# Performance work log

Measured on AMD Instinct MI355X. Metric: run time of the kernel, lower is better.

## Reference

```python
import jax, jax.numpy as jnp
import numpy as np

B, C, HK, WK = 1, 128, 32, 32
S = 4                       # upsample factor hq/hk = dilation
HQ, WQ = HK * S, WK * S
NH = 4                      # heads
HD = C // NH                # head dim
KH = KW = 7                 # odd(max(3, round(2*0.1*32)))
DH = DW = S
EPS = float(jnp.finfo(jnp.float32).eps)  # torch RMSNorm default eps for fp32


def natten_indices(L, K, D):
    """NATTEN clamped-window key indices per query position. Returns [L, K] int array."""
    NS = K // 2
    i = np.arange(L)
    if D <= 1:
        start = np.maximum(i - NS, 0) + (i + NS >= L) * (L - i - NS - 1)
    else:
        ni = i - NS * D
        imodd = i % D
        a = (L // D) * D
        b = L - a
        far = np.where(imodd < b, L - b + imodd - 2 * NS * D, a + imodd - K * D)
        start = np.where(ni < 0, imodd, np.where(i + NS * D >= L, far, ni))
    return jnp.asarray(start[:, None] + np.arange(K)[None, :] * D)


def setup_inputs() -> dict:
    key = jax.random.key(0)
    ks = jax.random.split(key, 8)
    sc = 1.0 / np.sqrt(C)
    return {
        "q": jax.random.normal(ks[0], (B, C, HQ, WQ), jnp.float32),
        "k": jax.random.normal(ks[1], (B, C, HK, WK), jnp.float32),
        "v": jax.random.normal(ks[2], (B, C, HK, WK), jnp.float32),
        "conv_w": jax.random.normal(ks[3], (C, C, 3, 3), jnp.float32) * (sc / 3.0),
        "normq_w": 1.0 + 0.02 * jax.random.normal(ks[4], (C,), jnp.float32),
        "normk_w": 1.0 + 0.02 * jax.random.normal(ks[5], (C,), jnp.float32),
        "qproj_w": jax.random.normal(ks[6], (C, C), jnp.float32) * sc,
        "qproj_b": jnp.zeros((C,), jnp.float32),
        "kproj_w": jax.random.normal(ks[7], (C, C), jnp.float32) * sc,
        "kproj_b": jnp.zeros((C,), jnp.float32),
    }


def _rmsnorm(x, w):  # x: [B,C,H,W]; RMS over channel dim
    ms = jnp.mean(x * x, axis=1, keepdims=True)
    return x * jax.lax.rsqrt(ms + EPS) * w[None, :, None, None]


def reference(q, k, v, conv_w, normq_w, normk_w, qproj_w, qproj_b, kproj_w, kproj_b):
    # 3x3 conv on q (no bias, padding=1)
    q = jax.lax.conv_general_dilated(q, conv_w, (1, 1), "SAME",
                                     dimension_numbers=("NCHW", "OIHW", "NCHW"))
    q = _rmsnorm(q, normq_w)
    k = _rmsnorm(k, normk_w)
    # 1x1 projections (Conv2d k=1 with bias)
    q = jnp.einsum("oc,bchw->bohw", qproj_w, q) + qproj_b[None, :, None, None]
    k = jnp.einsum("oc,bchw->bohw", kproj_w, k) + kproj_b[None, :, None, None]
    # nearest-exact upsample of k, v to (HQ, WQ); integer factor -> exact pixel repeat
    k = jnp.repeat(jnp.repeat(k, S, axis=2), S, axis=3)
    v = jnp.repeat(jnp.repeat(v, S, axis=2), S, axis=3)
    # NATTEN layout [B, H, W, heads, hd]
    qn = q.reshape(B, NH, HD, HQ, WQ).transpose(0, 3, 4, 1, 2)
    kn = k.reshape(B, NH, HD, HQ, WQ).transpose(0, 3, 4, 1, 2)
    vh = v.transpose(0, 2, 3, 1)  # [B,HQ,WQ,C]; V is shared (expanded) across heads.
    # channel-pad-to-8 in the original is a no-op here since C % 8 == 0.
    ih = natten_indices(HQ, KH, DH)  # [HQ, KH]
    iw = natten_indices(WQ, KW, DW)  # [WQ, KW]
    k_nb = jnp.take(jnp.take(kn, ih, axis=1), iw, axis=3)  # [B,HQ,KH,WQ,KW,NH,HD]
    v_nb = jnp.take(jnp.take(vh, ih, axis=1), iw, axis=3)  # [B,HQ,KH,WQ,KW,C]
    scale = HD ** -0.5
    logits = jnp.einsum("bijhd,bimjnhd->bijhmn", qn, k_nb) * scale
    attn = jax.nn.softmax(logits.reshape(B, HQ, WQ, NH, KH * KW), axis=-1)
    attn = attn.reshape(B, HQ, WQ, NH, KH, KW)
    # heads share V, and the block takes mean over heads at the end; the mean
    # commutes with the (linear) V-contraction, so average attention first.
    attn_mean = attn.mean(axis=3)  # [B,HQ,WQ,KH,KW]
    out = jnp.einsum("bijmn,bimjnc->bcij", attn_mean, v_nb)  # [B,C,HQ,WQ]
    return out
```

## Files before the change

### kernel.cpp

```cpp
#include <hip/hip_runtime.h>

#define EPS_ 1.1920928955078125e-07f
#define SCALE_ 0.17677669529663687f

typedef __attribute__((ext_vector_type(8))) short s8b;
typedef __attribute__((ext_vector_type(4))) float f32x4;

static __device__ __forceinline__ unsigned short f2bf(float f) {
  unsigned int u = __float_as_uint(f);
  unsigned int r = (u + 0x7fffu + ((u >> 16) & 1u)) >> 16;
  return (unsigned short)r;
}
static __device__ __forceinline__ float b2fs(short h) {
  return __uint_as_float(((unsigned int)(unsigned short)h) << 16);
}
static __device__ __forceinline__ int S_(int c) {
  return (c < 3) ? 0 : ((c > 28) ? 25 : (c - 3));
}

__global__ __launch_bounds__(256) void prep_k(
    const float* __restrict__ q_in, const float* __restrict__ k_in,
    const float* __restrict__ v_in, const float* __restrict__ conv_w,
    const float* __restrict__ normq_w, const float* __restrict__ normk_w,
    const float* __restrict__ qproj_w, const float* __restrict__ kproj_w,
    const float* __restrict__ kbias,
    unsigned short* __restrict__ qb, unsigned short* __restrict__ vb,
    unsigned short* __restrict__ kpb, unsigned short* __restrict__ wb,
    unsigned short* __restrict__ wnq) {
  __shared__ __align__(16) char smem[53504];
  unsigned short* t_l = (unsigned short*)smem;
  unsigned short* x_l = (unsigned short*)smem;
  unsigned short* wnk_l = (unsigned short*)(smem + 17408);
  float* red_l = (float*)(smem + 52224);
  float* rs_l  = (float*)(smem + 53248);
  const int b = blockIdx.x, tid = threadIdx.x;
  const int w = tid >> 6, lane = tid & 63;
  const int lm = lane & 15, kg = lane >> 4;

  if (b < 256 || (b >= 265 && b < 281)) {
    const float* src = (b < 256) ? q_in : v_in;
    const int N = (b < 256) ? 16384 : 1024;
    const int px0 = (b < 256) ? b * 64 : (b - 265) * 64;
    for (int i = tid; i < 2048; i += 256) {
      int c = i >> 4, f = i & 15;
      float4 v = *(const float4*)&src[c * N + px0 + f * 4];
      t_l[(f * 4 + 0) * 136 + c] = f2bf(v.x);
      t_l[(f * 4 + 1) * 136 + c] = f2bf(v.y);
      t_l[(f * 4 + 2) * 136 + c] = f2bf(v.z);
      t_l[(f * 4 + 3) * 136 + c] = f2bf(v.w);
    }
    __syncthreads();
    if (b < 256) {
      for (int i = tid; i < 1024; i += 256) {
        int p = i >> 4, s = i & 15;
        int px = px0 + p;
        int opx = px + 2 * (px >> 7) + 131;
        *(s8b*)&qb[opx * 128 + s * 8] = *(const s8b*)&t_l[p * 136 + s * 8];
      }
    } else {
      for (int i = tid; i < 1024; i += 256) {
        int p = i >> 4, s = i & 15;
        *(s8b*)&vb[(px0 + p) * 128 + s * 8] = *(const s8b*)&t_l[p * 136 + s * 8];
      }
    }
  } else if (b < 265) {
    int gid = (b - 256) * 256 + tid;
    s8b z = {0, 0, 0, 0, 0, 0, 0, 0};
    for (int j = gid; j < 2080; j += 2304) {
      *(s8b*)&qb[j * 8] = z;
      *(s8b*)&qb[129 * 130 * 128 + j * 8] = z;
    }
    for (int j = gid; j < 2048; j += 2304) {
      int r = (j >> 4) + 1, s = j & 15;
      *(s8b*)&qb[(r * 130) * 128 + s * 8] = z;
      *(s8b*)&qb[(r * 130 + 129) * 128 + s * 8] = z;
    }
  } else if (b < 297) {
    const int px0 = (b - 281) * 64;
    for (int i = tid; i < 2048; i += 256) {
      int c = i >> 4, f = i & 15;
      float4 v = *(const float4*)&k_in[c * 1024 + px0 + f * 4];
      x_l[(f * 4 + 0) * 136 + c] = f2bf(v.x);
      x_l[(f * 4 + 1) * 136 + c] = f2bf(v.y);
      x_l[(f * 4 + 2) * 136 + c] = f2bf(v.z);
      x_l[(f * 4 + 3) * 136 + c] = f2bf(v.w);
    }
    for (int i = tid; i < 16384; i += 256) {
      int o = i >> 7, c = i & 127;
      wnk_l[o * 136 + c] = f2bf(kproj_w[i] * normk_w[c]);
    }
    __syncthreads();
    {
      int px = tid >> 2, t4 = tid & 3;
      float ssum = 0.f;
#pragma unroll
      for (int j = 0; j < 4; j++) {
        s8b v = *(const s8b*)&x_l[px * 136 + t4 * 32 + j * 8];
#pragma unroll
        for (int e = 0; e < 8; e++) { float f = b2fs(v[e]); ssum += f * f; }
      }
      red_l[px * 4 + t4] = ssum;
    }
    __syncthreads();
    if (tid < 64)
      rs_l[tid] = rsqrtf((red_l[4 * tid] + red_l[4 * tid + 1] + red_l[4 * tid + 2] +
                          red_l[4 * tid + 3]) * (1.f / 128.f) + EPS_);
    __syncthreads();
    f32x4 acc[2][4];
#pragma unroll
    for (int a = 0; a < 2; a++)
#pragma unroll
      for (int n = 0; n < 4; n++) acc[a][n] = (f32x4){0.f, 0.f, 0.f, 0.f};
#pragma unroll
    for (int kc = 0; kc < 4; kc++) {
      s8b a0 = *(const s8b*)&wnk_l[(2 * w * 16 + lm) * 136 + kc * 32 + kg * 8];
      s8b a1 = *(const s8b*)&wnk_l[((2 * w + 1) * 16 + lm) * 136 + kc * 32 + kg * 8];
#pragma unroll
      for (int nt = 0; nt < 4; nt++) {
        s8b bf = *(const s8b*)&x_l[(nt * 16 + lm) * 136 + kc * 32 + kg * 8];
        acc[0][nt] = __builtin_amdgcn_mfma_f32_16x16x32_bf16(a0, bf, acc[0][nt], 0, 0, 0);
        acc[1][nt] = __builtin_amdgcn_mfma_f32_16x16x32_bf16(a1, bf, acc[1][nt], 0, 0, 0);
      }
    }
    __syncthreads();
#pragma unroll
    for (int mi = 0; mi < 2; mi++)
#pragma unroll
      for (int nt = 0; nt < 4; nt++)
#pragma unroll
        for (int r = 0; r < 4; r++) {
          int px = nt * 16 + lm, c = (2 * w + mi) * 16 + kg * 4 + r;
          x_l[px * 136 + c] = f2bf(kbias[c] + rs_l[px] * acc[mi][nt][r]);
        }
    __syncthreads();
    for (int i = tid; i < 1024; i += 256) {
      int px = i >> 4, s = i & 15;
      *(s8b*)&kpb[(px0 + px) * 128 + s * 8] = *(const s8b*)&x_l[px * 136 + s * 8];
    }
  } else {
    int idx = (b - 297) * 256 + tid;
    if (idx < 147456) {
      int i32 = idx & 31, r = idx >> 5;
      int oc = r & 127, r2 = r >> 7;
      int kc = r2 & 3, t = r2 >> 2;
      wb[idx] = f2bf(conv_w[oc * 1152 + (kc * 32 + i32) * 9 + t]);
    } else {
      int j = idx - 147456;
      wnq[j] = f2bf(qproj_w[j] * normq_w[j & 127]);
    }
  }
}

__global__ __launch_bounds__(256) void fused_k(
    const unsigned short* __restrict__ qb, const unsigned short* __restrict__ wb,
    const unsigned short* __restrict__ wnq, const float* __restrict__ qbias,
    const unsigned short* __restrict__ kpb, const unsigned short* __restrict__ vb,
    float* __restrict__ out) {
  __shared__ __align__(16) char smem[54528];
  unsigned short* in_l = (unsigned short*)smem;
  unsigned short* qc_l = (unsigned short*)smem;
  unsigned short* a_l  = (unsigned short*)smem;
  float* o_l = (float*)smem;
  unsigned short* v_l = (unsigned short*)(smem + 34816);
  float* red_l = (float*)(smem + 53248);
  float* rs_l  = (float*)(smem + 54272);

  const int tid = threadIdx.x;
  const int CY = blockIdx.x >> 4, CX = blockIdx.x & 15;
  const int Y0 = CY * 8, X0 = CX * 8;
  const int w = tid >> 6, lane = tid & 63;
  const int lm = lane & 15, kg = lane >> 4;

  const int sy0 = S_(2 * CY), sy1 = S_(2 * CY + 1);
  const int sx0 = S_(2 * CX), sx1 = S_(2 * CX + 1);
  const int kyb = min(sy0, 24), kxb = min(sx0, 24);
  const int oy0 = sy0 - kyb, oy1 = sy1 - kyb;
  const int ox0 = sx0 - kxb, ox1 = sx1 - kxb;

  for (int i = tid; i < 1600; i += 256) {
    int s = i & 15, r = i >> 4;
    int ry = r / 10, rx = r - ry * 10;
    *(s8b*)&in_l[(ry * 12 + rx) * 136 + s * 8] =
        *(const s8b*)&qb[((Y0 + ry) * 130 + X0 + rx) * 128 + s * 8];
  }
  for (int i = tid; i < 1024; i += 256) {
    int j = i >> 4, s = i & 15;
    int ky = j >> 3, kx = j & 7;
    s8b v = *(const s8b*)&vb[((kyb + ky) * 32 + kxb + kx) * 128 + s * 8];
#pragma unroll
    for (int e = 0; e < 8; e++) v_l[(s * 8 + e) * 72 + j] = (unsigned short)v[e];
  }
  __syncthreads();

  f32x4 acc[2][4];
#pragma unroll
  for (int a = 0; a < 2; a++)
#pragma unroll
    for (int n = 0; n < 4; n++) acc[a][n] = (f32x4){0.f, 0.f, 0.f, 0.f};
#pragma unroll
  for (int t = 0; t < 9; t++) {
    const int dy = t / 3, dx = t - (t / 3) * 3;
#pragma unroll
    for (int kc = 0; kc < 4; kc++) {
      const unsigned short* wp = wb + (t * 4 + kc) * 4096;
      s8b a0 = *(const s8b*)&wp[(2 * w * 16 + lm) * 32 + kg * 8];
      s8b a1 = *(const s8b*)&wp[((2 * w + 1) * 16 + lm) * 32 + kg * 8];
#pragma unroll
      for (int nt = 0; nt < 4; nt++) {
        int qy = 2 * nt + (lm >> 3), qx = lm & 7;
        s8b bf = *(const s8b*)&in_l[((qy + dy) * 12 + qx + dx) * 136 + kc * 32 + kg * 8];
        acc[0][nt] = __builtin_amdgcn_mfma_f32_16x16x32_bf16(a0, bf, acc[0][nt], 0, 0, 0);
        acc[1][nt] = __builtin_amdgcn_mfma_f32_16x16x32_bf16(a1, bf, acc[1][nt], 0, 0, 0);
      }
    }
  }
  __syncthreads();
#pragma unroll
  for (int mi = 0; mi < 2; mi++)
#pragma unroll
    for (int nt = 0; nt < 4; nt++)
#pragma unroll
      for (int r = 0; r < 4; r++) {
        int px = nt * 16 + lm, c = (2 * w + mi) * 16 + kg * 4 + r;
        qc_l[px * 136 + c] = f2bf(acc[mi][nt][r]);
      }
  __syncthreads();

  {
    int px = tid >> 2, t4 = tid & 3;
    float ssum = 0.f;
#pragma unroll
    for (int j = 0; j < 4; j++) {
      s8b v = *(const s8b*)&qc_l[px * 136 + t4 * 32 + j * 8];
#pragma unroll
      for (int e = 0; e < 8; e++) { float f = b2fs(v[e]); ssum += f * f; }
    }
    red_l[px * 4 + t4] = ssum;
  }
  __syncthreads();
  if (tid < 64)
    rs_l[tid] = rsqrtf((red_l[4 * tid] + red_l[4 * tid + 1] + red_l[4 * tid + 2] +
                        red_l[4 * tid + 3]) * (1.f / 128.f) + EPS_);
  __syncthreads();

  f32x4 acc2[2][4];
#pragma unroll
  for (int a = 0; a < 2; a++)
#pragma unroll
    for (int n = 0; n < 4; n++) acc2[a][n] = (f32x4){0.f, 0.f, 0.f, 0.f};
#pragma unroll
  for (int kc = 0; kc < 4; kc++) {
    s8b a0 = *(const s8b*)&wnq[(2 * w * 16 + lm) * 128 + kc * 32 + kg * 8];
    s8b a1 = *(const s8b*)&wnq[((2 * w + 1) * 16 + lm) * 128 + kc * 32 + kg * 8];
#pragma unroll
    for (int nt = 0; nt < 4; nt++) {
      s8b bf = *(const s8b*)&qc_l[(nt * 16 + lm) * 136 + kc * 32 + kg * 8];
      acc2[0][nt] = __builtin_amdgcn_mfma_f32_16x16x32_bf16(a0, bf, acc2[0][nt], 0, 0, 0);
      acc2[1][nt] = __builtin_amdgcn_mfma_f32_16x16x32_bf16(a1, bf, acc2[1][nt], 0, 0, 0);
    }
  }
  __syncthreads();
#pragma unroll
  for (int mi = 0; mi < 2; mi++)
#pragma unroll
    for (int nt = 0; nt < 4; nt++)
#pragma unroll
      for (int r = 0; r < 4; r++) {
        int px = nt * 16 + lm, c = (2 * w + mi) * 16 + kg * 4 + r;
        qc_l[px * 136 + c] = f2bf(qbias[c] + rs_l[px] * acc2[mi][nt][r]);
      }
  __syncthreads();

  const int h = w;
  f32x4 lg[4][4];
  {
    s8b af[4], bf[4];
#pragma unroll
    for (int mt = 0; mt < 4; mt++)
      af[mt] = *(const s8b*)&qc_l[(mt * 16 + lm) * 136 + h * 32 + kg * 8];
#pragma unroll
    for (int nt = 0; nt < 4; nt++) {
      int n = nt * 16 + lm;
      int ky = n >> 3, kx = n & 7;
      bf[nt] = *(const s8b*)&kpb[((kyb + ky) * 32 + kxb + kx) * 128 + h * 32 + kg * 8];
    }
#pragma unroll
    for (int mt = 0; mt < 4; mt++)
#pragma unroll
      for (int nt = 0; nt < 4; nt++)
        lg[mt][nt] = __builtin_amdgcn_mfma_f32_16x16x32_bf16(
            af[mt], bf[nt], (f32x4){0.f, 0.f, 0.f, 0.f}, 0, 0, 0);
  }
  __syncthreads();

  const int kyA = lm >> 3, kxq = lm & 7;
  const bool kxv0 = (unsigned)(kxq - ox0) < 7u;
  const bool kxv1 = (unsigned)(kxq - ox1) < 7u;
#pragma unroll
  for (int mt = 0; mt < 4; mt++) {
#pragma unroll
    for (int r = 0; r < 4; r++) {
      int j = mt * 16 + kg * 4 + r;
      int oy = ((j >> 5) & 1) ? oy1 : oy0;
      bool kxv = ((j >> 2) & 1) ? kxv1 : kxv0;
      float l[4];
#pragma unroll
      for (int nt = 0; nt < 4; nt++) {
        int ky = 2 * nt + kyA;
        bool valid = kxv && ((unsigned)(ky - oy) < 7u);
        l[nt] = valid ? lg[mt][nt][r] * SCALE_ : -1e30f;
      }
      float mx = fmaxf(fmaxf(l[0], l[1]), fmaxf(l[2], l[3]));
#pragma unroll
      for (int off = 1; off < 16; off <<= 1) mx = fmaxf(mx, __shfl_xor(mx, off, 64));
      float e0 = __expf(l[0] - mx), e1 = __expf(l[1] - mx);
      float e2 = __expf(l[2] - mx), e3 = __expf(l[3] - mx);
      float ss = e0 + e1 + e2 + e3;
#pragma unroll
      for (int off = 1; off < 16; off <<= 1) ss += __shfl_xor(ss, off, 64);
      float inv = 1.f / ss;
      unsigned short* ap = &a_l[(h * 64 + j) * 68];
      ap[lm] = f2bf(e0 * inv);
      ap[16 + lm] = f2bf(e1 * inv);
      ap[32 + lm] = f2bf(e2 * inv);
      ap[48 + lm] = f2bf(e3 * inv);
    }
  }
  __syncthreads();

  f32x4 oacc[4][2];
#pragma unroll
  for (int a = 0; a < 4; a++)
#pragma unroll
    for (int n = 0; n < 2; n++) oacc[a][n] = (f32x4){0.f, 0.f, 0.f, 0.f};
#pragma unroll
  for (int kc = 0; kc < 2; kc++) {
    s8b bfr[2];
#pragma unroll
    for (int nt2 = 0; nt2 < 2; nt2++)
      bfr[nt2] = *(const s8b*)&v_l[(w * 32 + nt2 * 16 + lm) * 72 + kc * 32 + kg * 8];
#pragma unroll
    for (int hh = 0; hh < 4; hh++) {
#pragma unroll
      for (int mt = 0; mt < 4; mt++) {
        s8b afr = *(const s8b*)&a_l[(hh * 64 + mt * 16 + lm) * 68 + kc * 32 + kg * 8];
#pragma unroll
        for (int nt2 = 0; nt2 < 2; nt2++)
          oacc[mt][nt2] = __builtin_amdgcn_mfma_f32_16x16x32_bf16(afr, bfr[nt2], oacc[mt][nt2], 0, 0, 0);
      }
    }
  }
  __syncthreads();
#pragma unroll
  for (int mt = 0; mt < 4; mt++)
#pragma unroll
    for (int nt2 = 0; nt2 < 2; nt2++)
#pragma unroll
      for (int r = 0; r < 4; r++)
        o_l[(w * 32 + nt2 * 16 + lm) * 68 + mt * 16 + kg * 4 + r] = 0.25f * oacc[mt][nt2][r];
  __syncthreads();
  for (int i = tid; i < 2048; i += 256) {
    int c = i >> 4, rr = i & 15;
    int qy = rr >> 1, hx = rr & 1;
    float4 v = *(const float4*)&o_l[c * 68 + qy * 8 + hx * 4];
    *(float4*)&out[c * 16384 + (Y0 + qy) * 128 + X0 + hx * 4] = v;
  }
}

extern "C" void kernel_launch(void* const* d_in, const int* in_sizes, int n_in,
                              void* d_out, int out_size, void* d_ws, size_t ws_size,
                              hipStream_t stream) {
  const float* q_in    = (const float*)d_in[0];
  const float* k_in    = (const float*)d_in[1];
  const float* v_in    = (const float*)d_in[2];
  const float* conv_w  = (const float*)d_in[3];
  const float* normq_w = (const float*)d_in[4];
  const float* normk_w = (const float*)d_in[5];
  const float* qproj_w = (const float*)d_in[6];
  const float* qproj_b = (const float*)d_in[7];
  const float* kproj_w = (const float*)d_in[8];
  const float* kproj_b = (const float*)d_in[9];
  float* out = (float*)d_out;

  char* ws = (char*)d_ws;
  unsigned short* qb  = (unsigned short*)(ws);
  unsigned short* vb  = (unsigned short*)(ws + 4326400);
  unsigned short* kpb = (unsigned short*)(ws + 4588544);
  unsigned short* wb  = (unsigned short*)(ws + 4850688);
  unsigned short* wnq = (unsigned short*)(ws + 5145600);

  prep_k<<<dim3(937), 256, 0, stream>>>(q_in, k_in, v_in, conv_w, normq_w, normk_w,
                                        qproj_w, kproj_w, kproj_b,
                                        qb, vb, kpb, wb, wnq);
  fused_k<<<dim3(256), 256, 0, stream>>>(qb, wb, wnq, qproj_b, kpb, vb, out);
}
```

Measured before the change: 114.0 us.

## Double fused kernel threads to 512 and restructure prep kernel conversions

The fused kernel now runs 8 waves per block instead of 4. The conv and projection GEMMs are split across a 2x2 wave grid, the attention work is split by head and query half, and the PV product is split by pixel half and channel block. The prep kernel stores V channel-major with a direct vectorized conversion instead of a transpose, and writes conv weights with coalesced 9-way stores. The V tile load in the fused kernel becomes vector copies with an odd-offset shift. The aim is more latency hiding per CU and fewer prep blocks, at the cost of more registers and sync pressure per block.

```diff
diff --git a/kernel.cpp b/kernel.cpp
--- a/kernel.cpp
+++ b/kernel.cpp
@@ -37,31 +37,22 @@
   const int w = tid >> 6, lane = tid & 63;
   const int lm = lane & 15, kg = lane >> 4;
 
-  if (b < 256 || (b >= 265 && b < 281)) {
-    const float* src = (b < 256) ? q_in : v_in;
-    const int N = (b < 256) ? 16384 : 1024;
-    const int px0 = (b < 256) ? b * 64 : (b - 265) * 64;
+  if (b < 256) {
+    const int px0 = b * 64;
     for (int i = tid; i < 2048; i += 256) {
       int c = i >> 4, f = i & 15;
-      float4 v = *(const float4*)&src[c * N + px0 + f * 4];
+      float4 v = *(const float4*)&q_in[c * 16384 + px0 + f * 4];
       t_l[(f * 4 + 0) * 136 + c] = f2bf(v.x);
       t_l[(f * 4 + 1) * 136 + c] = f2bf(v.y);
       t_l[(f * 4 + 2) * 136 + c] = f2bf(v.z);
       t_l[(f * 4 + 3) * 136 + c] = f2bf(v.w);
     }
     __syncthreads();
-    if (b < 256) {
-      for (int i = tid; i < 1024; i += 256) {
-        int p = i >> 4, s = i & 15;
-        int px = px0 + p;
-        int opx = px + 2 * (px >> 7) + 131;
-        *(s8b*)&qb[opx * 128 + s * 8] = *(const s8b*)&t_l[p * 136 + s * 8];
-      }
-    } else {
-      for (int i = tid; i < 1024; i += 256) {
-        int p = i >> 4, s = i & 15;
-        *(s8b*)&vb[(px0 + p) * 128 + s * 8] = *(const s8b*)&t_l[p * 136 + s * 8];
-      }
+    for (int i = tid; i < 1024; i += 256) {
+      int p = i >> 4, s = i & 15;
+      int px = px0 + p;
+      int opx = px + 2 * (px >> 7) + 131;
+      *(s8b*)&qb[opx * 128 + s * 8] = *(const s8b*)&t_l[p * 136 + s * 8];
     }
   } else if (b < 265) {
     int gid = (b - 256) * 256 + tid;
@@ -75,8 +66,21 @@
       *(s8b*)&qb[(r * 130) * 128 + s * 8] = z;
       *(s8b*)&qb[(r * 130 + 129) * 128 + s * 8] = z;
     }
-  } else if (b < 297) {
-    const int px0 = (b - 281) * 64;
+  } else if (b < 269) {
+#pragma unroll
+    for (int it = 0; it < 16; it++) {
+      int ch8 = (b - 265) * 4096 + it * 256 + tid;
+      const float4 v0 = *(const float4*)&v_in[ch8 * 8];
+      const float4 v1 = *(const float4*)&v_in[ch8 * 8 + 4];
+      s8b o;
+      o[0] = (short)f2bf(v0.x); o[1] = (short)f2bf(v0.y);
+      o[2] = (short)f2bf(v0.z); o[3] = (short)f2bf(v0.w);
+      o[4] = (short)f2bf(v1.x); o[5] = (short)f2bf(v1.y);
+      o[6] = (short)f2bf(v1.z); o[7] = (short)f2bf(v1.w);
+      *(s8b*)&vb[ch8 * 8] = o;
+    }
+  } else if (b < 285) {
+    const int px0 = (b - 269) * 64;
     for (int i = tid; i < 2048; i += 256) {
       int c = i >> 4, f = i & 15;
       float4 v = *(const float4*)&k_in[c * 1024 + px0 + f * 4];
@@ -137,39 +141,47 @@
       int px = i >> 4, s = i & 15;
       *(s8b*)&kpb[(px0 + px) * 128 + s * 8] = *(const s8b*)&x_l[px * 136 + s * 8];
     }
+  } else if (b < 349) {
+    int g = (b - 285) * 256 + tid;
+    int i32 = g & 31, oc = (g >> 5) & 127, kc = g >> 12;
+    const float* src = conv_w + oc * 1152 + (kc * 32 + i32) * 9;
+#pragma unroll
+    for (int t = 0; t < 9; t++)
+      wb[t * 16384 + g] = f2bf(src[t]);
   } else {
-    int idx = (b - 297) * 256 + tid;
-    if (idx < 147456) {
-      int i32 = idx & 31, r = idx >> 5;
-      int oc = r & 127, r2 = r >> 7;
-      int kc = r2 & 3, t = r2 >> 2;
-      wb[idx] = f2bf(conv_w[oc * 1152 + (kc * 32 + i32) * 9 + t]);
-    } else {
-      int j = idx - 147456;
-      wnq[j] = f2bf(qproj_w[j] * normq_w[j & 127]);
-    }
-  }
-}
-
-__global__ __launch_bounds__(256) void fused_k(
+    int base = ((b - 349) * 256 + tid) * 8;
+    const float4 v0 = *(const float4*)&qproj_w[base];
+    const float4 v1 = *(const float4*)&qproj_w[base + 4];
+    int c = base & 127;
+    s8b o;
+    o[0] = (short)f2bf(v0.x * normq_w[c + 0]); o[1] = (short)f2bf(v0.y * normq_w[c + 1]);
+    o[2] = (short)f2bf(v0.z * normq_w[c + 2]); o[3] = (short)f2bf(v0.w * normq_w[c + 3]);
+    o[4] = (short)f2bf(v1.x * normq_w[c + 4]); o[5] = (short)f2bf(v1.y * normq_w[c + 5]);
+    o[6] = (short)f2bf(v1.z * normq_w[c + 6]); o[7] = (short)f2bf(v1.w * normq_w[c + 7]);
+    *(s8b*)&wnq[base] = o;
+  }
+}
+
+__global__ __launch_bounds__(512) void fused_k(
     const unsigned short* __restrict__ qb, const unsigned short* __restrict__ wb,
     const unsigned short* __restrict__ wnq, const float* __restrict__ qbias,
     const unsigned short* __restrict__ kpb, const unsigned short* __restrict__ vb,
     float* __restrict__ out) {
-  __shared__ __align__(16) char smem[54528];
+  __shared__ __align__(16) char smem[55552];
   unsigned short* in_l = (unsigned short*)smem;
   unsigned short* qc_l = (unsigned short*)smem;
   unsigned short* a_l  = (unsigned short*)smem;
   float* o_l = (float*)smem;
   unsigned short* v_l = (unsigned short*)(smem + 34816);
   float* red_l = (float*)(smem + 53248);
-  float* rs_l  = (float*)(smem + 54272);
+  float* rs_l  = (float*)(smem + 55296);
 
   const int tid = threadIdx.x;
   const int CY = blockIdx.x >> 4, CX = blockIdx.x & 15;
   const int Y0 = CY * 8, X0 = CX * 8;
   const int w = tid >> 6, lane = tid & 63;
   const int lm = lane & 15, kg = lane >> 4;
+  const int wm = w >> 1, wn = w & 1;
 
   const int sy0 = S_(2 * CY), sy1 = S_(2 * CY + 1);
   const int sx0 = S_(2 * CX), sx1 = S_(2 * CX + 1);
@@ -177,40 +189,52 @@
   const int oy0 = sy0 - kyb, oy1 = sy1 - kyb;
   const int ox0 = sx0 - kxb, ox1 = sx1 - kxb;
 
-  for (int i = tid; i < 1600; i += 256) {
+  for (int i = tid; i < 1600; i += 512) {
     int s = i & 15, r = i >> 4;
     int ry = r / 10, rx = r - ry * 10;
     *(s8b*)&in_l[(ry * 12 + rx) * 136 + s * 8] =
         *(const s8b*)&qb[((Y0 + ry) * 130 + X0 + rx) * 128 + s * 8];
   }
-  for (int i = tid; i < 1024; i += 256) {
-    int j = i >> 4, s = i & 15;
-    int ky = j >> 3, kx = j & 7;
-    s8b v = *(const s8b*)&vb[((kyb + ky) * 32 + kxb + kx) * 128 + s * 8];
-#pragma unroll
-    for (int e = 0; e < 8; e++) v_l[(s * 8 + e) * 72 + j] = (unsigned short)v[e];
-  }
-  __syncthreads();
-
-  f32x4 acc[2][4];
+  {
+    const int kxe = kxb & ~1;
+    for (int i = tid; i < 1024; i += 512) {
+      int ch = i & 127, ky = i >> 7;
+      const unsigned short* src = &vb[ch * 1024 + (kyb + ky) * 32 + kxe];
+      s8b a = *(const s8b*)src;
+      if (kxb & 1) {
+        s8b bsec = *(const s8b*)(src + 8);
+        s8b o;
+#pragma unroll
+        for (int e = 0; e < 7; e++) o[e] = a[e + 1];
+        o[7] = bsec[0];
+        *(s8b*)&v_l[ch * 72 + ky * 8] = o;
+      } else {
+        *(s8b*)&v_l[ch * 72 + ky * 8] = a;
+      }
+    }
+  }
+  __syncthreads();
+
+  f32x4 acc[2][2];
 #pragma unroll
   for (int a = 0; a < 2; a++)
 #pragma unroll
-    for (int n = 0; n < 4; n++) acc[a][n] = (f32x4){0.f, 0.f, 0.f, 0.f};
+    for (int n = 0; n < 2; n++) acc[a][n] = (f32x4){0.f, 0.f, 0.f, 0.f};
 #pragma unroll
   for (int t = 0; t < 9; t++) {
     const int dy = t / 3, dx = t - (t / 3) * 3;
 #pragma unroll
     for (int kc = 0; kc < 4; kc++) {
       const unsigned short* wp = wb + (t * 4 + kc) * 4096;
-      s8b a0 = *(const s8b*)&wp[(2 * w * 16 + lm) * 32 + kg * 8];
-      s8b a1 = *(const s8b*)&wp[((2 * w + 1) * 16 + lm) * 32 + kg * 8];
-#pragma unroll
-      for (int nt = 0; nt < 4; nt++) {
+      s8b a0 = *(const s8b*)&wp[(wm * 32 + lm) * 32 + kg * 8];
+      s8b a1 = *(const s8b*)&wp[(wm * 32 + 16 + lm) * 32 + kg * 8];
+#pragma unroll
+      for (int ni = 0; ni < 2; ni++) {
+        int nt = wn * 2 + ni;
         int qy = 2 * nt + (lm >> 3), qx = lm & 7;
         s8b bf = *(const s8b*)&in_l[((qy + dy) * 12 + qx + dx) * 136 + kc * 32 + kg * 8];
-        acc[0][nt] = __builtin_amdgcn_mfma_f32_16x16x32_bf16(a0, bf, acc[0][nt], 0, 0, 0);
-        acc[1][nt] = __builtin_amdgcn_mfma_f32_16x16x32_bf16(a1, bf, acc[1][nt], 0, 0, 0);
+        acc[0][ni] = __builtin_amdgcn_mfma_f32_16x16x32_bf16(a0, bf, acc[0][ni], 0, 0, 0);
+        acc[1][ni] = __builtin_amdgcn_mfma_f32_16x16x32_bf16(a1, bf, acc[1][ni], 0, 0, 0);
       }
     }
   }
@@ -218,78 +242,81 @@
 #pragma unroll
   for (int mi = 0; mi < 2; mi++)
 #pragma unroll
-    for (int nt = 0; nt < 4; nt++)
+    for (int ni = 0; ni < 2; ni++)
 #pragma unroll
       for (int r = 0; r < 4; r++) {
-        int px = nt * 16 + lm, c = (2 * w + mi) * 16 + kg * 4 + r;
-        qc_l[px * 136 + c] = f2bf(acc[mi][nt][r]);
+        int px = (wn * 2 + ni) * 16 + lm, c = wm * 32 + mi * 16 + kg * 4 + r;
+        qc_l[px * 136 + c] = f2bf(acc[mi][ni][r]);
       }
   __syncthreads();
 
   {
-    int px = tid >> 2, t4 = tid & 3;
+    int px = tid >> 3, t8 = tid & 7;
     float ssum = 0.f;
 #pragma unroll
-    for (int j = 0; j < 4; j++) {
-      s8b v = *(const s8b*)&qc_l[px * 136 + t4 * 32 + j * 8];
+    for (int j = 0; j < 2; j++) {
+      s8b v = *(const s8b*)&qc_l[px * 136 + t8 * 16 + j * 8];
 #pragma unroll
       for (int e = 0; e < 8; e++) { float f = b2fs(v[e]); ssum += f * f; }
     }
-    red_l[px * 4 + t4] = ssum;
-  }
-  __syncthreads();
-  if (tid < 64)
-    rs_l[tid] = rsqrtf((red_l[4 * tid] + red_l[4 * tid + 1] + red_l[4 * tid + 2] +
-                        red_l[4 * tid + 3]) * (1.f / 128.f) + EPS_);
-  __syncthreads();
-
-  f32x4 acc2[2][4];
+    red_l[px * 8 + t8] = ssum;
+  }
+  __syncthreads();
+  if (tid < 64) {
+    float4 r0 = *(const float4*)&red_l[tid * 8];
+    float4 r1 = *(const float4*)&red_l[tid * 8 + 4];
+    rs_l[tid] = rsqrtf((r0.x + r0.y + r0.z + r0.w + r1.x + r1.y + r1.z + r1.w) *
+                           (1.f / 128.f) + EPS_);
+  }
+  __syncthreads();
+
+  f32x4 acc2[2][2];
 #pragma unroll
   for (int a = 0; a < 2; a++)
 #pragma unroll
-    for (int n = 0; n < 4; n++) acc2[a][n] = (f32x4){0.f, 0.f, 0.f, 0.f};
+    for (int n = 0; n < 2; n++) acc2[a][n] = (f32x4){0.f, 0.f, 0.f, 0.f};
 #pragma unroll
   for (int kc = 0; kc < 4; kc++) {
-    s8b a0 = *(const s8b*)&wnq[(2 * w * 16 + lm) * 128 + kc * 32 + kg * 8];
-    s8b a1 = *(const s8b*)&wnq[((2 * w + 1) * 16 + lm) * 128 + kc * 32 + kg * 8];
-#pragma unroll
-    for (int nt = 0; nt < 4; nt++) {
-      s8b bf = *(const s8b*)&qc_l[(nt * 16 + lm) * 136 + kc * 32 + kg * 8];
-      acc2[0][nt] = __builtin_amdgcn_mfma_f32_16x16x32_bf16(a0, bf, acc2[0][nt], 0, 0, 0);
-      acc2[1][nt] = __builtin_amdgcn_mfma_f32_16x16x32_bf16(a1, bf, acc2[1][nt], 0, 0, 0);
+    s8b a0 = *(const s8b*)&wnq[(wm * 32 + lm) * 128 + kc * 32 + kg * 8];
+    s8b a1 = *(const s8b*)&wnq[(wm * 32 + 16 + lm) * 128 + kc * 32 + kg * 8];
+#pragma unroll
+    for (int ni = 0; ni < 2; ni++) {
+      s8b bf = *(const s8b*)&qc_l[((wn * 2 + ni) * 16 + lm) * 136 + kc * 32 + kg * 8];
+      acc2[0][ni] = __builtin_amdgcn_mfma_f32_16x16x32_bf16(a0, bf, acc2[0][ni], 0, 0, 0);
+      acc2[1][ni] = __builtin_amdgcn_mfma_f32_16x16x32_bf16(a1, bf, acc2[1][ni], 0, 0, 0);
     }
   }
   __syncthreads();
 #pragma unroll
   for (int mi = 0; mi < 2; mi++)
 #pragma unroll
-    for (int nt = 0; nt < 4; nt++)
+    for (int ni = 0; ni < 2; ni++)
 #pragma unroll
       for (int r = 0; r < 4; r++) {
-        int px = nt * 16 + lm, c = (2 * w + mi) * 16 + kg * 4 + r;
-        qc_l[px * 136 + c] = f2bf(qbias[c] + rs_l[px] * acc2[mi][nt][r]);
-      }
-  __syncthreads();
-
-  const int h = w;
-  f32x4 lg[4][4];
+        int px = (wn * 2 + ni) * 16 + lm, c = wm * 32 + mi * 16 + kg * 4 + r;
+        qc_l[px * 136 + c] = f2bf(qbias[c] + rs_l[px] * acc2[mi][ni][r]);
+      }
+  __syncthreads();
+
+  const int h = w >> 1, qh = w & 1;
+  f32x4 lg[2][4];
   {
-    s8b af[4], bf[4];
-#pragma unroll
-    for (int mt = 0; mt < 4; mt++)
-      af[mt] = *(const s8b*)&qc_l[(mt * 16 + lm) * 136 + h * 32 + kg * 8];
+    s8b af[2], bfv[4];
+#pragma unroll
+    for (int i = 0; i < 2; i++)
+      af[i] = *(const s8b*)&qc_l[((qh * 2 + i) * 16 + lm) * 136 + h * 32 + kg * 8];
 #pragma unroll
     for (int nt = 0; nt < 4; nt++) {
       int n = nt * 16 + lm;
       int ky = n >> 3, kx = n & 7;
-      bf[nt] = *(const s8b*)&kpb[((kyb + ky) * 32 + kxb + kx) * 128 + h * 32 + kg * 8];
-    }
-#pragma unroll
-    for (int mt = 0; mt < 4; mt++)
+      bfv[nt] = *(const s8b*)&kpb[((kyb + ky) * 32 + kxb + kx) * 128 + h * 32 + kg * 8];
+    }
+#pragma unroll
+    for (int i = 0; i < 2; i++)
 #pragma unroll
       for (int nt = 0; nt < 4; nt++)
-        lg[mt][nt] = __builtin_amdgcn_mfma_f32_16x16x32_bf16(
-            af[mt], bf[nt], (f32x4){0.f, 0.f, 0.f, 0.f}, 0, 0, 0);
+        lg[i][nt] = __builtin_amdgcn_mfma_f32_16x16x32_bf16(
+            af[i], bfv[nt], (f32x4){0.f, 0.f, 0.f, 0.f}, 0, 0, 0);
   }
   __syncthreads();
 
@@ -297,7 +324,8 @@
   const bool kxv0 = (unsigned)(kxq - ox0) < 7u;
   const bool kxv1 = (unsigned)(kxq - ox1) < 7u;
 #pragma unroll
-  for (int mt = 0; mt < 4; mt++) {
+  for (int i = 0; i < 2; i++) {
+    const int mt = qh * 2 + i;
 #pragma unroll
     for (int r = 0; r < 4; r++) {
       int j = mt * 16 + kg * 4 + r;
@@ -308,7 +336,7 @@
       for (int nt = 0; nt < 4; nt++) {
         int ky = 2 * nt + kyA;
         bool valid = kxv && ((unsigned)(ky - oy) < 7u);
-        l[nt] = valid ? lg[mt][nt][r] * SCALE_ : -1e30f;
+        l[nt] = valid ? lg[i][nt][r] * SCALE_ : -1e30f;
       }
       float mx = fmaxf(fmaxf(l[0], l[1]), fmaxf(l[2], l[3]));
 #pragma unroll
@@ -328,9 +356,10 @@
   }
   __syncthreads();
 
-  f32x4 oacc[4][2];
-#pragma unroll
-  for (int a = 0; a < 4; a++)
+  const int ph = w & 1, cb = w >> 1;
+  f32x4 oacc[2][2];
+#pragma unroll
+  for (int a = 0; a < 2; a++)
 #pragma unroll
     for (int n = 0; n < 2; n++) oacc[a][n] = (f32x4){0.f, 0.f, 0.f, 0.f};
 #pragma unroll
@@ -338,28 +367,29 @@
     s8b bfr[2];
 #pragma unroll
     for (int nt2 = 0; nt2 < 2; nt2++)
-      bfr[nt2] = *(const s8b*)&v_l[(w * 32 + nt2 * 16 + lm) * 72 + kc * 32 + kg * 8];
+      bfr[nt2] = *(const s8b*)&v_l[(cb * 32 + nt2 * 16 + lm) * 72 + kc * 32 + kg * 8];
 #pragma unroll
     for (int hh = 0; hh < 4; hh++) {
 #pragma unroll
-      for (int mt = 0; mt < 4; mt++) {
-        s8b afr = *(const s8b*)&a_l[(hh * 64 + mt * 16 + lm) * 68 + kc * 32 + kg * 8];
+      for (int mi = 0; mi < 2; mi++) {
+        s8b afr = *(const s8b*)&a_l[(hh * 64 + (ph * 2 + mi) * 16 + lm) * 68 + kc * 32 + kg * 8];
 #pragma unroll
         for (int nt2 = 0; nt2 < 2; nt2++)
-          oacc[mt][nt2] = __builtin_amdgcn_mfma_f32_16x16x32_bf16(afr, bfr[nt2], oacc[mt][nt2], 0, 0, 0);
-      }
-    }
-  }
-  __syncthreads();
-#pragma unroll
-  for (int mt = 0; mt < 4; mt++)
+          oacc[mi][nt2] = __builtin_amdgcn_mfma_f32_16x16x32_bf16(afr, bfr[nt2], oacc[mi][nt2], 0, 0, 0);
+      }
+    }
+  }
+  __syncthreads();
+#pragma unroll
+  for (int mi = 0; mi < 2; mi++)
 #pragma unroll
     for (int nt2 = 0; nt2 < 2; nt2++)
 #pragma unroll
       for (int r = 0; r < 4; r++)
-        o_l[(w * 32 + nt2 * 16 + lm) * 68 + mt * 16 + kg * 4 + r] = 0.25f * oacc[mt][nt2][r];
-  __syncthreads();
-  for (int i = tid; i < 2048; i += 256) {
+        o_l[(cb * 32 + nt2 * 16 + lm) * 68 + (ph * 2 + mi) * 16 + kg * 4 + r] =
+            0.25f * oacc[mi][nt2][r];
+  __syncthreads();
+  for (int i = tid; i < 2048; i += 512) {
     int c = i >> 4, rr = i & 15;
     int qy = rr >> 1, hx = rr & 1;
     float4 v = *(const float4*)&o_l[c * 68 + qy * 8 + hx * 4];
@@ -389,8 +419,8 @@
   unsigned short* wb  = (unsigned short*)(ws + 4850688);
   unsigned short* wnq = (unsigned short*)(ws + 5145600);
 
-  prep_k<<<dim3(937), 256, 0, stream>>>(q_in, k_in, v_in, conv_w, normq_w, normk_w,
+  prep_k<<<dim3(357), 256, 0, stream>>>(q_in, k_in, v_in, conv_w, normq_w, normk_w,
                                         qproj_w, kproj_w, kproj_b,
                                         qb, vb, kpb, wb, wnq);
-  fused_k<<<dim3(256), 256, 0, stream>>>(qb, wb, wnq, qproj_b, kpb, vb, out);
-}
+  fused_k<<<dim3(256), 512, 0, stream>>>(qb, wb, wnq, qproj_b, kpb, vb, out);
+}
```

New measurement: 109.4 us. -4.1%, faster.
